# Performance work log

Hardware: AMD Instinct MI355X
Metric: run time of the kernel (lower is better)

The kernel has to match this reference:

```python
import jax, jax.numpy as jnp
import numpy as np

H = 16  # n_heads


def _ln(x, g, b, eps=1e-5):
    m = x.mean(-1, keepdims=True)
    v = ((x - m) ** 2).mean(-1, keepdims=True)
    return (x - m) / jnp.sqrt(v + eps) * g + b


def setup_inputs() -> dict:
    key = jax.random.key(0)
    ks = jax.random.split(key, 10)
    b, lq, d, dff, L = 2, 1024, 1024, 4096, 4
    s = 0.02
    return {
        "x": jax.random.normal(ks[0], (b, lq, d), jnp.float32),
        "memory_bank": jax.random.normal(ks[1], (L, b, lq, d), jnp.float32),
        "attn_mask": jax.random.bernoulli(ks[2], 0.3, (b, lq, lq)),
        "ln1_g": jnp.ones((d,), jnp.float32),
        "ln1_b": jnp.zeros((d,), jnp.float32),
        "Wq": jax.random.normal(ks[3], (d, d), jnp.float32) * s,
        "Wk": jax.random.normal(ks[4], (d, d), jnp.float32) * s,
        "Wv": jax.random.normal(ks[5], (d, d), jnp.float32) * s,
        "Wo": jax.random.normal(ks[6], (d, d), jnp.float32) * s,
        "ln2_g": jnp.ones((d,), jnp.float32),
        "ln2_b": jnp.zeros((d,), jnp.float32),
        "W1": jax.random.normal(ks[7], (d, dff), jnp.float32) * s,
        "b1": jnp.zeros((dff,), jnp.float32),
        "W2": jax.random.normal(ks[8], (dff, d), jnp.float32) * s,
        "b2": jnp.zeros((d,), jnp.float32),
    }


def reference(x, memory_bank, attn_mask, ln1_g, ln1_b, Wq, Wk, Wv, Wo,
              ln2_g, ln2_b, W1, b1, W2, b2):
    # x: [b, lq, d]; memory_bank: [L, b, lk, d]; attn_mask: [b, lq, lk] bool (True = masked)
    b, lq, d = x.shape
    dh = d // H
    # preprocess_attn: LayerNorm (eval mode -> dropouts are identity)
    q = _ln(x, ln1_g, ln1_b)
    # grow memory bank with current normalized input
    mem = jnp.concatenate([memory_bank, q[None]], axis=0)  # [L+1, b, lk, d]
    L, _, lk, _ = mem.shape
    # projections (bias-free); key/value projected per layer then flattened over (L, lk)
    pq = (q @ Wq).reshape(b, lq, H, dh).transpose(0, 2, 1, 3) * (dh ** -0.5)  # [b,h,lq,dh]
    pk = (mem @ Wk).transpose(1, 0, 2, 3).reshape(b, L * lk, H, dh).transpose(0, 2, 1, 3)
    pv = (mem @ Wv).transpose(1, 0, 2, 3).reshape(b, L * lk, H, dh).transpose(0, 2, 1, 3)
    scores = jnp.einsum('bhqd,bhkd->bhqk', pq, pk)           # [b,h,lq,L*lk]
    scores = scores.reshape(b, H, lq, L, lk)
    scores = jnp.where(attn_mask[:, None, :, None, :], -jnp.inf, scores)
    attn = jax.nn.softmax(scores.reshape(b, H, lq, L * lk), axis=-1)
    ctx = jnp.einsum('bhqk,bhkd->bhqd', attn, pv)            # [b,h,lq,dh]
    ctx = ctx.transpose(0, 2, 1, 3).reshape(b, lq, d)
    attn_out = ctx @ Wo
    # postprocess_attn: residual add
    x2 = x + attn_out
    # FFN: LayerNorm -> Linear -> ReLU -> Linear -> residual
    f = _ln(x2, ln2_g, ln2_b)
    f = jax.nn.relu(f @ W1 + b1) @ W2 + b2
    out = x2 + f
    return (out, mem)
```

## Files before the change

### kernel.cpp

```cpp
#include <hip/hip_runtime.h>
#include <hip/hip_bf16.h>

typedef __attribute__((ext_vector_type(8))) __bf16 bf16x8;
typedef __attribute__((ext_vector_type(4))) __bf16 bf16x4;
typedef __attribute__((ext_vector_type(4))) float f32x4;

#define MFMA16(a, b, c) __builtin_amdgcn_mfma_f32_16x16x32_bf16((a), (b), (c), 0, 0, 0)
#define LOG2E 1.4426950408889634f

static __device__ __forceinline__ float exp2_fast(float x) {
    float r; asm("v_exp_f32 %0, %1" : "=v"(r) : "v"(x)); return r;
}

__device__ __forceinline__ void gll16(const void* g, void* l) {
    __builtin_amdgcn_global_load_lds((const __attribute__((address_space(1))) void*)g,
                                     (__attribute__((address_space(3))) void*)l,
                                     16, 0, 0);
}

__global__ __launch_bounds__(256) void prep_kernel(const float* __restrict__ bank,
                                                   float* __restrict__ mem_out,
                                                   __bf16* __restrict__ membf,
                                                   const float* __restrict__ x,
                                                   const float* __restrict__ g,
                                                   const float* __restrict__ bta,
                                                   float* __restrict__ q_out,
                                                   __bf16* __restrict__ qbf) {
    __shared__ float rs[4], rs2[4];
    int blk = blockIdx.x;
    if (blk < 2048) {
        int i = blk * 256 + threadIdx.x;
        const float4* i4 = (const float4*)bank;
        float4* o4 = (float4*)mem_out;
        for (; i < 2097152; i += 2048 * 256) {
            float4 v = i4[i];
            o4[i] = v;
            if (membf) {
                bf16x4 ob = {(__bf16)v.x, (__bf16)v.y, (__bf16)v.z, (__bf16)v.w};
                ((bf16x4*)membf)[i] = ob;
            }
        }
    } else {
        int row = blk - 2048;
        const float4 v = ((const float4*)(x + (size_t)row * 1024))[threadIdx.x];
        float s = v.x + v.y + v.z + v.w;
        float s2 = v.x * v.x + v.y * v.y + v.z * v.z + v.w * v.w;
#pragma unroll
        for (int off = 1; off < 64; off <<= 1) {
            s += __shfl_xor(s, off);
            s2 += __shfl_xor(s2, off);
        }
        int wv = threadIdx.x >> 6;
        if ((threadIdx.x & 63) == 0) { rs[wv] = s; rs2[wv] = s2; }
        __syncthreads();
        s = rs[0] + rs[1] + rs[2] + rs[3];
        s2 = rs2[0] + rs2[1] + rs2[2] + rs2[3];
        float mean = s * (1.0f / 1024.0f);
        float var = s2 * (1.0f / 1024.0f) - mean * mean;
        float rstd = rsqrtf(var + 1e-5f);
        float4 gg = ((const float4*)g)[threadIdx.x];
        float4 bb = ((const float4*)bta)[threadIdx.x];
        float4 o;
        o.x = (v.x - mean) * rstd * gg.x + bb.x;
        o.y = (v.y - mean) * rstd * gg.y + bb.y;
        o.z = (v.z - mean) * rstd * gg.z + bb.z;
        o.w = (v.w - mean) * rstd * gg.w + bb.w;
        ((float4*)(q_out + (size_t)row * 1024))[threadIdx.x] = o;
        if (qbf) {
            bf16x4 ob = {(__bf16)o.x, (__bf16)o.y, (__bf16)o.z, (__bf16)o.w};
            ((bf16x4*)(qbf + (size_t)row * 1024))[threadIdx.x] = ob;
        }
    }
}

__global__ __launch_bounds__(256) void ln_kernel(const float* __restrict__ x,
                                                 const float* __restrict__ g,
                                                 const float* __restrict__ bta,
                                                 __bf16* __restrict__ outb) {
    int row = blockIdx.x;
    const float4 v = ((const float4*)(x + (size_t)row * 1024))[threadIdx.x];
    float s = v.x + v.y + v.z + v.w;
    float s2 = v.x * v.x + v.y * v.y + v.z * v.z + v.w * v.w;
#pragma unroll
    for (int off = 1; off < 64; off <<= 1) {
        s += __shfl_xor(s, off);
        s2 += __shfl_xor(s2, off);
    }
    __shared__ float rs[4], rs2[4];
    int wv = threadIdx.x >> 6;
    if ((threadIdx.x & 63) == 0) { rs[wv] = s; rs2[wv] = s2; }
    __syncthreads();
    s = rs[0] + rs[1] + rs[2] + rs[3];
    s2 = rs2[0] + rs2[1] + rs2[2] + rs2[3];
    float mean = s * (1.0f / 1024.0f);
    float var = s2 * (1.0f / 1024.0f) - mean * mean;
    float rstd = rsqrtf(var + 1e-5f);
    float4 gg = ((const float4*)g)[threadIdx.x];
    float4 bb = ((const float4*)bta)[threadIdx.x];
    bf16x4 ob;
    ob[0] = (__bf16)((v.x - mean) * rstd * gg.x + bb.x);
    ob[1] = (__bf16)((v.y - mean) * rstd * gg.y + bb.y);
    ob[2] = (__bf16)((v.z - mean) * rstd * gg.z + bb.z);
    ob[3] = (__bf16)((v.w - mean) * rstd * gg.w + bb.w);
    ((bf16x4*)(outb + (size_t)row * 1024))[threadIdx.x] = ob;
}

__device__ __forceinline__ void tr_body(const float* __restrict__ in, __bf16* __restrict__ out,
                                        int K, int N, int k0, int n0) {
    __shared__ float tile[32][33];
    int tx = threadIdx.x & 31, ty = threadIdx.x >> 5;
#pragma unroll
    for (int i = 0; i < 4; i++)
        tile[ty + i * 8][tx] = in[(size_t)(k0 + ty + i * 8) * N + n0 + tx];
    __syncthreads();
#pragma unroll
    for (int i = 0; i < 4; i++)
        out[(size_t)(n0 + ty + i * 8) * K + k0 + tx] = (__bf16)tile[tx][ty + i * 8];
}

__global__ __launch_bounds__(256) void tr_early(const float* __restrict__ Wq,
                                                const float* __restrict__ Wk,
                                                const float* __restrict__ Wv,
                                                __bf16* __restrict__ Wq_t,
                                                __bf16* __restrict__ Wkv_t) {
    int w = blockIdx.x;
    int sel = w >> 10, within = w & 1023;
    const float* in = (sel == 0) ? Wq : ((sel == 1) ? Wk : Wv);
    __bf16* out = (sel == 0) ? Wq_t : (Wkv_t + (size_t)(sel - 1) * 1048576);
    tr_body(in, out, 1024, 1024, (within >> 5) * 32, (within & 31) * 32);
}

__global__ __launch_bounds__(256) void tr_late(const float* __restrict__ Wo,
                                               const float* __restrict__ W1,
                                               const float* __restrict__ W2,
                                               __bf16* __restrict__ Wo_t,
                                               __bf16* __restrict__ W1_t,
                                               __bf16* __restrict__ W2_t) {
    int w = blockIdx.x;
    const float* in;
    __bf16* out;
    int K, N, k0, n0;
    if (w < 1024) {
        in = Wo; out = Wo_t; K = 1024; N = 1024; n0 = (w & 31) * 32; k0 = (w >> 5) * 32;
    } else if (w < 5120) {
        int v = w - 1024;
        in = W1; out = W1_t; K = 1024; N = 4096; n0 = (v & 127) * 32; k0 = (v >> 7) * 32;
    } else {
        int v = w - 5120;
        in = W2; out = W2_t; K = 4096; N = 1024; n0 = (v & 31) * 32; k0 = (v >> 5) * 32;
    }
    tr_body(in, out, K, N, k0, n0);
}

template <int EPI, bool ABF16>
__device__ __forceinline__ void gemm_core(const void* __restrict__ Av,
                                          const __bf16* __restrict__ Bt,
                                          void* __restrict__ Cout,
                                          const float* __restrict__ bias,
                                          const float* __restrict__ res,
                                          int N, int lda, int ldb, int klen,
                                          float scale, int bm, int bn) {
    constexpr int LDA = ABF16 ? 32 : 40;
    __shared__ __bf16 As[128 * LDA];
    __shared__ __bf16 Bs[128 * 32];

    int t = threadIdx.x;
    int lane = t & 63, wave = t >> 6;
    int wm = (wave >> 1) * 64, wn = (wave & 1) * 64;
    int l16 = lane & 15, l4 = lane >> 4;

    f32x4 acc[4][4];
#pragma unroll
    for (int m = 0; m < 4; m++)
#pragma unroll
        for (int n = 0; n < 4; n++) acc[m][n] = (f32x4){0.f, 0.f, 0.f, 0.f};

    int srow = t >> 2;
    int scol = (t & 3) * 8;
    int ar = t >> 1, ak = (t & 1) * 16;
    const __bf16* Ab = (const __bf16*)Av;
    const float* Af = (const float*)Av;

    for (int k0 = 0; k0 < klen; k0 += 32) {
        gll16(Bt + (size_t)(bn + srow) * ldb + (k0 + scol), &Bs[wave * 512]);
        gll16(Bt + (size_t)(bn + 64 + srow) * ldb + (k0 + scol), &Bs[2048 + wave * 512]);
        if constexpr (ABF16) {
            gll16(Ab + (size_t)(bm + srow) * lda + (k0 + scol), &As[wave * 512]);
            gll16(Ab + (size_t)(bm + 64 + srow) * lda + (k0 + scol), &As[2048 + wave * 512]);
        } else {
            const float* ap = Af + (size_t)(bm + ar) * lda + k0 + ak;
            float4 f0 = ((const float4*)ap)[0];
            float4 f1 = ((const float4*)ap)[1];
            float4 f2 = ((const float4*)ap)[2];
            float4 f3 = ((const float4*)ap)[3];
            float ta[16] = {f0.x, f0.y, f0.z, f0.w, f1.x, f1.y, f1.z, f1.w,
                            f2.x, f2.y, f2.z, f2.w, f3.x, f3.y, f3.z, f3.w};
            bf16x8 v0, v1;
#pragma unroll
            for (int j = 0; j < 8; j++) { v0[j] = (__bf16)ta[j]; v1[j] = (__bf16)ta[j + 8]; }
            *(bf16x8*)&As[ar * 40 + ak] = v0;
            *(bf16x8*)&As[ar * 40 + ak + 8] = v1;
        }
        __syncthreads();

        bf16x8 af[4], bfr[4];
#pragma unroll
        for (int m = 0; m < 4; m++) af[m] = *(const bf16x8*)&As[(wm + m * 16 + l16) * LDA + l4 * 8];
#pragma unroll
        for (int n = 0; n < 4; n++) bfr[n] = *(const bf16x8*)&Bs[(wn + n * 16 + l16) * 32 + l4 * 8];
#pragma unroll
        for (int m = 0; m < 4; m++)
#pragma unroll
            for (int n = 0; n < 4; n++) acc[m][n] = MFMA16(af[m], bfr[n], acc[m][n]);
        __syncthreads();
    }

#pragma unroll
    for (int m = 0; m < 4; m++) {
#pragma unroll
        for (int r = 0; r < 4; r++) {
            int row = bm + wm + m * 16 + l4 * 4 + r;
#pragma unroll
            for (int n = 0; n < 4; n++) {
                int col = bn + wn + n * 16 + l16;
                float c = acc[m][n][r];
                size_t idx = (size_t)row * N + col;
                if (EPI == 0) {
                    ((__bf16*)Cout)[idx] = (__bf16)(c * scale);
                } else if (EPI == 1) {
                    ((float*)Cout)[idx] = c + res[idx];
                } else if (EPI == 2) {
                    ((__bf16*)Cout)[idx] = (__bf16)fmaxf(c + bias[col], 0.0f);
                } else if (EPI == 3) {
                    ((float*)Cout)[idx] = c + bias[col] + res[idx];
                } else {
                    ((float*)Cout)[idx] = c;
                }
            }
        }
    }
}

template <int EPI, bool ABF16>
__global__ __launch_bounds__(256) void gemm_bt(const void* __restrict__ Av,
                                               const __bf16* __restrict__ Bt,
                                               void* __restrict__ Cout,
                                               const float* __restrict__ bias,
                                               const float* __restrict__ res,
                                               int N, int K, float scale, int nbx) {
    int q = gridDim.x >> 3;
    int swz = (blockIdx.x & 7) * q + (blockIdx.x >> 3);
    int bn = (swz % nbx) * 128;
    int bm = (swz / nbx) * 128;
    gemm_core<EPI, ABF16>(Av, Bt, Cout, bias, res, N, K, K, K, scale, bm, bn);
}

template <bool ABF16>
__global__ __launch_bounds__(256) void gemm_proj(const void* __restrict__ Akv,
                                                 const __bf16* __restrict__ Wkv_t,
                                                 __bf16* __restrict__ PKV,
                                                 const void* __restrict__ Aq,
                                                 const __bf16* __restrict__ Wq_t,
                                                 __bf16* __restrict__ Pq) {
    int q = gridDim.x >> 3;
    int swz = (blockIdx.x & 7) * q + (blockIdx.x >> 3);
    const void* A;
    const __bf16* B;
    __bf16* C;
    int N, bm, bn;
    float sc;
    if (swz < 1280) {
        A = Akv; B = Wkv_t; C = PKV; N = 2048; sc = 1.0f;
        bn = (swz & 15) * 128; bm = (swz >> 4) * 128;
    } else {
        int p = swz - 1280;
        A = Aq; B = Wq_t; C = Pq; N = 1024; sc = 0.125f * LOG2E;
        bn = (p & 7) * 128; bm = (p >> 3) * 128;
    }
    gemm_core<0, ABF16>(A, B, C, nullptr, nullptr, N, 1024, 1024, 1024, sc, bm, bn);
}

__global__ __launch_bounds__(256) void gemm_w2(const __bf16* __restrict__ h1,
                                               const __bf16* __restrict__ W2_t,
                                               float* __restrict__ pc0,
                                               float* __restrict__ pc1) {
    int q = gridDim.x >> 3;
    int swz = (blockIdx.x & 7) * q + (blockIdx.x >> 3);
    int half = swz >> 7;
    int p = swz & 127;
    int bn = (p & 7) * 128, bm = (p >> 3) * 128;
    int koff = half * 2048;
    gemm_core<4, true>(h1 + koff, W2_t + koff, half ? pc1 : pc0, nullptr, nullptr,
                       1024, 4096, 4096, 2048, 1.0f, bm, bn);
}

__global__ __launch_bounds__(256) void w2comb(const float* __restrict__ pc0,
                                              const float* __restrict__ pc1,
                                              const float* __restrict__ b2,
                                              const float* __restrict__ x2,
                                              float* __restrict__ out) {
    int i = blockIdx.x * 256 + threadIdx.x;
    float4 a = ((const float4*)pc0)[i];
    float4 b = ((const float4*)pc1)[i];
    float4 r = ((const float4*)x2)[i];
    float4 bb = ((const float4*)b2)[i & 255];
    float4 o;
    o.x = a.x + b.x + r.x + bb.x;
    o.y = a.y + b.y + r.y + bb.y;
    o.z = a.z + b.z + r.z + bb.z;
    o.w = a.w + b.w + r.w + bb.w;
    ((float4*)out)[i] = o;
}

#define LKV 5120
#define KHALF 2560
#define CK 64
#define NCH 40
__global__ __launch_bounds__(512, 4) void attn_kernel(const __bf16* __restrict__ Pq,
                                                      const __bf16* __restrict__ PKV,
                                                      const unsigned char* __restrict__ mask,
                                                      __bf16* __restrict__ ctx) {
    int bh = blockIdx.x;
    int b = bh >> 4, h = bh & 15;
    int wave = threadIdx.x >> 6, lane = threadIdx.x & 63;
    int grp = wave >> 2, wv = wave & 3;
    int l16 = lane & 15, l4 = lane >> 4;
    int q0 = blockIdx.y * 64 + wv * 16;

    __shared__ __bf16 Ks[2][64][72];
    __shared__ __bf16 Vt[2][64][72];
    __shared__ __bf16 Ps[8][16][72];

    const f32x4 fzero = {0.f, 0.f, 0.f, 0.f};

    bf16x8 qf[2];
    {
        const __bf16* pqrow = Pq + (size_t)(b * 1024 + q0 + l16) * 1024 + h * 64;
        qf[0] = *(const bf16x8*)(pqrow + l4 * 8);
        qf[1] = *(const bf16x8*)(pqrow + 32 + l4 * 8);
    }

    f32x4 accT[4];
#pragma unroll
    for (int n = 0; n < 4; n++) accT[n] = fzero;
    float m = 0.0f;
    float lsum = 0.0f;

    const unsigned char* mrow_p = mask + (size_t)b * (1024u * 1024u) + (size_t)(q0 + l16) * 1024;

    int tl = threadIdx.x & 255;
    int skey = tl >> 2;
    int sd0 = (tl & 3) << 4;
    int kgbase = grp * KHALF;

    bf16x8 rk0, rk1, rv0, rv1;
    unsigned int mk[4], mkn[4];
    {
        int kg = kgbase + skey;
        int lidx = kg >> 10, i = kg & 1023;
        size_t off = ((size_t)(lidx * 2048 + b * 1024 + i) << 11) + h * 64 + sd0;
        rk0 = *(const bf16x8*)(PKV + off);
        rk1 = *(const bf16x8*)(PKV + off + 8);
        rv0 = *(const bf16x8*)(PKV + off + 1024);
        rv1 = *(const bf16x8*)(PKV + off + 1032);
        int kloc = kgbase & 1023;
#pragma unroll
        for (int tile = 0; tile < 4; tile++)
            mk[tile] = *(const unsigned int*)(mrow_p + kloc + tile * 16 + l4 * 4);
    }

    for (int t = 0; t < NCH; t++) {
        *(bf16x8*)&Ks[grp][skey][sd0] = rk0;
        *(bf16x8*)&Ks[grp][skey][sd0 + 8] = rk1;
#pragma unroll
        for (int j = 0; j < 8; j++) {
            int row = sd0 + j;
            Vt[grp][row][skey ^ ((row >> 3) << 3)] = rv0[j];
            int row2 = sd0 + 8 + j;
            Vt[grp][row2][skey ^ ((row2 >> 3) << 3)] = rv1[j];
        }
        __syncthreads();

        if (t + 1 < NCH) {
            int kg = kgbase + (t + 1) * CK + skey;
            int lidx = kg >> 10, i = kg & 1023;
            size_t off = ((size_t)(lidx * 2048 + b * 1024 + i) << 11) + h * 64 + sd0;
            rk0 = *(const bf16x8*)(PKV + off);
            rk1 = *(const bf16x8*)(PKV + off + 8);
            rv0 = *(const bf16x8*)(PKV + off + 1024);
            rv1 = *(const bf16x8*)(PKV + off + 1032);
            int kloc = (kgbase + (t + 1) * CK) & 1023;
#pragma unroll
            for (int tile = 0; tile < 4; tile++)
                mkn[tile] = *(const unsigned int*)(mrow_p + kloc + tile * 16 + l4 * 4);
        }

        f32x4 s[4];
        __builtin_amdgcn_s_setprio(1);
#pragma unroll
        for (int tile = 0; tile < 4; tile++) {
            bf16x8 ka = *(const bf16x8*)&Ks[grp][tile * 16 + l16][l4 * 8];
            bf16x8 kb = *(const bf16x8*)&Ks[grp][tile * 16 + l16][32 + l4 * 8];
            f32x4 sz = fzero;
            sz = MFMA16(ka, qf[0], sz);
            sz = MFMA16(kb, qf[1], sz);
            s[tile] = sz;
        }
        __builtin_amdgcn_s_setprio(0);

        float pa = fmaxf(fmaxf(s[0][0], s[0][1]), fmaxf(s[0][2], s[0][3]));
        float pb = fmaxf(fmaxf(s[1][0], s[1][1]), fmaxf(s[1][2], s[1][3]));
        float pc = fmaxf(fmaxf(s[2][0], s[2][1]), fmaxf(s[2][2], s[2][3]));
        float pd = fmaxf(fmaxf(s[3][0], s[3][1]), fmaxf(s[3][2], s[3][3]));
        float pmax = fmaxf(fmaxf(pa, pb), fmaxf(pc, pd));
        pmax = fmaxf(pmax, __shfl_xor(pmax, 16));
        pmax = fmaxf(pmax, __shfl_xor(pmax, 32));
        if (__builtin_expect(pmax > m + 8.0f, 0)) {
            float sc = exp2_fast(m - pmax);
            lsum *= sc;
#pragma unroll
            for (int n = 0; n < 4; n++) accT[n] *= sc;
            m = pmax;
        }
        float psum = 0.0f;
#pragma unroll
        for (int tile = 0; tile < 4; tile++) {
            bf16x4 pk_;
#pragma unroll
            for (int r = 0; r < 4; r++) {
                float e = exp2_fast(s[tile][r] - m);
                e = ((mk[tile] >> (r * 8)) & 255u) ? 0.0f : e;
                psum += e;
                pk_[r] = (__bf16)e;
            }
            *(bf16x4*)&Ps[wave][l16][tile * 16 + l4 * 4] = pk_;
        }
        lsum += psum;
#pragma unroll
        for (int tile = 0; tile < 4; tile++) mk[tile] = mkn[tile];

        __builtin_amdgcn_s_setprio(1);
#pragma unroll
        for (int kk = 0; kk < 2; kk++) {
            bf16x8 pf = *(const bf16x8*)&Ps[wave][l16][kk * 32 + l4 * 8];
#pragma unroll
            for (int n = 0; n < 4; n++) {
                int row = n * 16 + l16;
                int colblk = (kk * 32 + l4 * 8) ^ ((row >> 3) << 3);
                bf16x8 vf = *(const bf16x8*)&Vt[grp][row][colblk];
                accT[n] = MFMA16(vf, pf, accT[n]);
            }
        }
        __builtin_amdgcn_s_setprio(0);
        __syncthreads();
    }

    lsum += __shfl_xor(lsum, 16);
    lsum += __shfl_xor(lsum, 32);

    float* exAcc = (float*)&Ks[0][0][0];
    float* exM = (float*)&Vt[0][0][0];
    float* exL = exM + 64;
    if (grp == 1) {
#pragma unroll
        for (int n = 0; n < 4; n++)
            *(f32x4*)&exAcc[(wv * 16 + l16) * 68 + n * 16 + l4 * 4] = accT[n];
        if (l4 == 0) { exM[wv * 16 + l16] = m; exL[wv * 16 + l16] = lsum; }
    }
    __syncthreads();
    if (grp == 0) {
        int qi = wv * 16 + l16;
        float m1 = exM[qi], l1 = exL[qi];
        float M = fmaxf(m, m1);
        float e0 = exp2_fast(m - M), e1 = exp2_fast(m1 - M);
        float inv = 1.0f / (lsum * e0 + l1 * e1);
        __bf16* crow = ctx + ((size_t)(b * 1024 + q0 + l16) << 10) + h * 64;
#pragma unroll
        for (int n = 0; n < 4; n++) {
            f32x4 a1 = *(const f32x4*)&exAcc[qi * 68 + n * 16 + l4 * 4];
            bf16x4 o;
#pragma unroll
            for (int r = 0; r < 4; r++) o[r] = (__bf16)((accT[n][r] * e0 + a1[r] * e1) * inv);
            *(bf16x4*)&crow[n * 16 + l4 * 4] = o;
        }
    }
}

extern "C" void kernel_launch(void* const* d_in, const int* in_sizes, int n_in,
                              void* d_out, int out_size, void* d_ws, size_t ws_size,
                              hipStream_t stream) {
    const float* x = (const float*)d_in[0];
    const float* memory_bank = (const float*)d_in[1];
    const unsigned char* attn_mask = (const unsigned char*)d_in[2];
    const float* ln1_g = (const float*)d_in[3];
    const float* ln1_b = (const float*)d_in[4];
    const float* Wq = (const float*)d_in[5];
    const float* Wk = (const float*)d_in[6];
    const float* Wv = (const float*)d_in[7];
    const float* Wo = (const float*)d_in[8];
    const float* ln2_g = (const float*)d_in[9];
    const float* ln2_b = (const float*)d_in[10];
    const float* W1 = (const float*)d_in[11];
    const float* b1 = (const float*)d_in[12];
    const float* W2 = (const float*)d_in[13];
    const float* b2 = (const float*)d_in[14];

    float* out = (float*)d_out;
    float* mem_out = out + 2097152;
    float* q_out = mem_out + 4 * 2097152;

    char* ws = (char*)d_ws;
    bool big = ws_size >= (70ull << 20);

    __bf16* PKV = (__bf16*)ws;
    __bf16 *Pq, *Wq_t, *Wkv_t, *ctx, *membf = nullptr, *qbf = nullptr;
    if (big) {
        membf = (__bf16*)(ws + (40ull << 20));
        qbf = membf + (size_t)8192 * 1024;
        Wq_t = (__bf16*)(ws + (60ull << 20));
        Wkv_t = (__bf16*)(ws + (62ull << 20));
        Pq = (__bf16*)(ws + (66ull << 20));
        ctx = (__bf16*)(ws + (60ull << 20));
    } else {
        Pq = (__bf16*)(ws + (40ull << 20));
        Wq_t = (__bf16*)(ws + (44ull << 20));
        Wkv_t = (__bf16*)(ws + (46ull << 20));
        ctx = (__bf16*)(ws + (44ull << 20));
    }
    __bf16* Wo_t = (__bf16*)ws;
    __bf16* W1_t = (__bf16*)(ws + (2ull << 20));
    __bf16* W2_t = (__bf16*)(ws + (10ull << 20));
    float* x2 = (float*)(ws + (18ull << 20));
    __bf16* fln = (__bf16*)(ws + (26ull << 20));
    __bf16* h1 = (__bf16*)(ws + (30ull << 20));
    float* pc0 = (float*)(ws + (46ull << 20));
    float* pc1 = (float*)(ws + (54ull << 20));

    prep_kernel<<<4096, 256, 0, stream>>>(memory_bank, mem_out, membf, x, ln1_g, ln1_b,
                                          q_out, qbf);
    tr_early<<<3072, 256, 0, stream>>>(Wq, Wk, Wv, Wq_t, Wkv_t);

    if (big)
        gemm_proj<true><<<1408, 256, 0, stream>>>(membf, Wkv_t, PKV, qbf, Wq_t, Pq);
    else
        gemm_proj<false><<<1408, 256, 0, stream>>>(mem_out, Wkv_t, PKV, q_out, Wq_t, Pq);

    attn_kernel<<<dim3(32, 16), 512, 0, stream>>>(Pq, PKV, attn_mask, ctx);

    tr_late<<<9216, 256, 0, stream>>>(Wo, W1, W2, Wo_t, W1_t, W2_t);

    gemm_bt<1, true><<<128, 256, 0, stream>>>(ctx, Wo_t, x2, nullptr, x, 1024, 1024, 1.0f, 8);
    ln_kernel<<<2048, 256, 0, stream>>>(x2, ln2_g, ln2_b, fln);
    gemm_bt<2, true><<<512, 256, 0, stream>>>(fln, W1_t, h1, b1, nullptr, 4096, 1024, 1.0f, 32);
    if (big) {
        gemm_w2<<<256, 256, 0, stream>>>(h1, W2_t, pc0, pc1);
        w2comb<<<2048, 256, 0, stream>>>(pc0, pc1, b2, x2, out);
    } else {
        gemm_bt<3, true><<<128, 256, 0, stream>>>(h1, W2_t, out, b2, x2, 1024, 4096, 1.0f, 8);
    }
}
```

Baseline: 301.7 us.

## Double-buffer attention K/V tiles with XOR swizzle and split-K the Wo GEMM

The attention kernel now keeps two LDS buffers for K and transposed V. The next chunk is written to LDS while the current one is consumed, so only one barrier per iteration is needed instead of two. Padding is replaced by XOR swizzles on the K, V and P tiles to avoid bank conflicts, and the global pointer advance is made incremental. The Wo projection is split into two K-halves writing fp32 partials, which a generalized combine kernel adds with the residual. This doubles the Wo grid for better CU occupancy but adds an extra pass over memory.

```diff
diff --git a/kernel.cpp b/kernel.cpp
--- a/kernel.cpp
+++ b/kernel.cpp
@@ -294,21 +294,38 @@
                        1024, 4096, 4096, 2048, 1.0f, bm, bn);
 }
 
-__global__ __launch_bounds__(256) void w2comb(const float* __restrict__ pc0,
-                                              const float* __restrict__ pc1,
-                                              const float* __restrict__ b2,
-                                              const float* __restrict__ x2,
-                                              float* __restrict__ out) {
+__global__ __launch_bounds__(256) void gemm_wo(const __bf16* __restrict__ ctx,
+                                               const __bf16* __restrict__ Wo_t,
+                                               float* __restrict__ pc0,
+                                               float* __restrict__ pc1) {
+    int q = gridDim.x >> 3;
+    int swz = (blockIdx.x & 7) * q + (blockIdx.x >> 3);
+    int half = swz >> 7;
+    int p = swz & 127;
+    int bn = (p & 7) * 128, bm = (p >> 3) * 128;
+    int koff = half * 512;
+    gemm_core<4, true>(ctx + koff, Wo_t + koff, half ? pc1 : pc0, nullptr, nullptr,
+                       1024, 1024, 1024, 512, 1.0f, bm, bn);
+}
+
+__global__ __launch_bounds__(256) void comb_kernel(const float* __restrict__ pc0,
+                                                   const float* __restrict__ pc1,
+                                                   const float* __restrict__ bias,
+                                                   const float* __restrict__ res,
+                                                   float* __restrict__ out) {
     int i = blockIdx.x * 256 + threadIdx.x;
     float4 a = ((const float4*)pc0)[i];
     float4 b = ((const float4*)pc1)[i];
-    float4 r = ((const float4*)x2)[i];
-    float4 bb = ((const float4*)b2)[i & 255];
+    float4 r = ((const float4*)res)[i];
     float4 o;
-    o.x = a.x + b.x + r.x + bb.x;
-    o.y = a.y + b.y + r.y + bb.y;
-    o.z = a.z + b.z + r.z + bb.z;
-    o.w = a.w + b.w + r.w + bb.w;
+    o.x = a.x + b.x + r.x;
+    o.y = a.y + b.y + r.y;
+    o.z = a.z + b.z + r.z;
+    o.w = a.w + b.w + r.w;
+    if (bias) {
+        float4 bb = ((const float4*)bias)[i & 255];
+        o.x += bb.x; o.y += bb.y; o.z += bb.z; o.w += bb.w;
+    }
     ((float4*)out)[i] = o;
 }
 
@@ -316,6 +333,8 @@
 #define KHALF 2560
 #define CK 64
 #define NCH 40
+#define KSW(r, c) ((c) ^ (((r) & 7) << 3))
+#define VSW(r, c) ((c) ^ ((((r) >> 3) & 7) << 3))
 __global__ __launch_bounds__(512, 4) void attn_kernel(const __bf16* __restrict__ Pq,
                                                       const __bf16* __restrict__ PKV,
                                                       const unsigned char* __restrict__ mask,
@@ -327,9 +346,9 @@
     int l16 = lane & 15, l4 = lane >> 4;
     int q0 = blockIdx.y * 64 + wv * 16;
 
-    __shared__ __bf16 Ks[2][64][72];
-    __shared__ __bf16 Vt[2][64][72];
-    __shared__ __bf16 Ps[8][16][72];
+    __shared__ __bf16 Ks[2][2][64][64];
+    __shared__ __bf16 Vt[2][2][64][64];
+    __shared__ __bf16 Ps[8][16][64];
 
     const f32x4 fzero = {0.f, 0.f, 0.f, 0.f};
 
@@ -353,54 +372,73 @@
     int sd0 = (tl & 3) << 4;
     int kgbase = grp * KHALF;
 
+    int kmod = kgbase & 1023;
+    const __bf16* pkv = PKV + (((size_t)((kgbase >> 10) * 2048 + b * 1024 + kmod + skey)) << 11)
+                        + h * 64 + sd0;
     bf16x8 rk0, rk1, rv0, rv1;
     unsigned int mk[4], mkn[4];
-    {
-        int kg = kgbase + skey;
-        int lidx = kg >> 10, i = kg & 1023;
-        size_t off = ((size_t)(lidx * 2048 + b * 1024 + i) << 11) + h * 64 + sd0;
-        rk0 = *(const bf16x8*)(PKV + off);
-        rk1 = *(const bf16x8*)(PKV + off + 8);
-        rv0 = *(const bf16x8*)(PKV + off + 1024);
-        rv1 = *(const bf16x8*)(PKV + off + 1032);
-        int kloc = kgbase & 1023;
-#pragma unroll
-        for (int tile = 0; tile < 4; tile++)
-            mk[tile] = *(const unsigned int*)(mrow_p + kloc + tile * 16 + l4 * 4);
-    }
+
+    rk0 = *(const bf16x8*)(pkv);
+    rk1 = *(const bf16x8*)(pkv + 8);
+    rv0 = *(const bf16x8*)(pkv + 1024);
+    rv1 = *(const bf16x8*)(pkv + 1032);
+    { int st = (kmod + CK >= 1024) ? (CK + 1024) : CK; kmod = (kmod + CK) & 1023; pkv += (size_t)st << 11; }
+    int kloc0 = kgbase & 1023;
+#pragma unroll
+    for (int tile = 0; tile < 4; tile++)
+        mk[tile] = *(const unsigned int*)(mrow_p + kloc0 + tile * 16 + l4 * 4);
+    int kloc_m = (kloc0 + CK) & 1023;
+
+    *(bf16x8*)&Ks[grp][0][skey][KSW(skey, sd0)] = rk0;
+    *(bf16x8*)&Ks[grp][0][skey][KSW(skey, sd0 + 8)] = rk1;
+#pragma unroll
+    for (int j = 0; j < 8; j++) {
+        int r1 = sd0 + j, r2 = sd0 + 8 + j;
+        Vt[grp][0][r1][VSW(r1, skey)] = rv0[j];
+        Vt[grp][0][r2][VSW(r2, skey)] = rv1[j];
+    }
+    rk0 = *(const bf16x8*)(pkv);
+    rk1 = *(const bf16x8*)(pkv + 8);
+    rv0 = *(const bf16x8*)(pkv + 1024);
+    rv1 = *(const bf16x8*)(pkv + 1032);
+    { int st = (kmod + CK >= 1024) ? (CK + 1024) : CK; kmod = (kmod + CK) & 1023; pkv += (size_t)st << 11; }
 
     for (int t = 0; t < NCH; t++) {
-        *(bf16x8*)&Ks[grp][skey][sd0] = rk0;
-        *(bf16x8*)&Ks[grp][skey][sd0 + 8] = rk1;
-#pragma unroll
-        for (int j = 0; j < 8; j++) {
-            int row = sd0 + j;
-            Vt[grp][row][skey ^ ((row >> 3) << 3)] = rv0[j];
-            int row2 = sd0 + 8 + j;
-            Vt[grp][row2][skey ^ ((row2 >> 3) << 3)] = rv1[j];
-        }
+        int cb = t & 1, nb = cb ^ 1;
         __syncthreads();
-
         if (t + 1 < NCH) {
-            int kg = kgbase + (t + 1) * CK + skey;
-            int lidx = kg >> 10, i = kg & 1023;
-            size_t off = ((size_t)(lidx * 2048 + b * 1024 + i) << 11) + h * 64 + sd0;
-            rk0 = *(const bf16x8*)(PKV + off);
-            rk1 = *(const bf16x8*)(PKV + off + 8);
-            rv0 = *(const bf16x8*)(PKV + off + 1024);
-            rv1 = *(const bf16x8*)(PKV + off + 1032);
-            int kloc = (kgbase + (t + 1) * CK) & 1023;
+            *(bf16x8*)&Ks[grp][nb][skey][KSW(skey, sd0)] = rk0;
+            *(bf16x8*)&Ks[grp][nb][skey][KSW(skey, sd0 + 8)] = rk1;
+#pragma unroll
+            for (int j = 0; j < 8; j++) {
+                int r1 = sd0 + j, r2 = sd0 + 8 + j;
+                Vt[grp][nb][r1][VSW(r1, skey)] = rv0[j];
+                Vt[grp][nb][r2][VSW(r2, skey)] = rv1[j];
+            }
+        }
+        if (t + 2 < NCH) {
+            rk0 = *(const bf16x8*)(pkv);
+            rk1 = *(const bf16x8*)(pkv + 8);
+            rv0 = *(const bf16x8*)(pkv + 1024);
+            rv1 = *(const bf16x8*)(pkv + 1032);
+            int st = (kmod + CK >= 1024) ? (CK + 1024) : CK;
+            kmod = (kmod + CK) & 1023;
+            pkv += (size_t)st << 11;
+        }
+        if (t + 1 < NCH) {
 #pragma unroll
             for (int tile = 0; tile < 4; tile++)
-                mkn[tile] = *(const unsigned int*)(mrow_p + kloc + tile * 16 + l4 * 4);
+                mkn[tile] = *(const unsigned int*)(mrow_p + kloc_m + tile * 16 + l4 * 4);
+            kloc_m = (kloc_m + CK) & 1023;
         }
 
         f32x4 s[4];
         __builtin_amdgcn_s_setprio(1);
 #pragma unroll
         for (int tile = 0; tile < 4; tile++) {
-            bf16x8 ka = *(const bf16x8*)&Ks[grp][tile * 16 + l16][l4 * 8];
-            bf16x8 kb = *(const bf16x8*)&Ks[grp][tile * 16 + l16][32 + l4 * 8];
+            int row = tile * 16 + l16;
+            bf16x8 ka = *(const bf16x8*)&Ks[grp][cb][row][KSW(row, l4 * 8)];
+            bf16x8 kb = *(const bf16x8*)&Ks[grp][cb][row][KSW(row, 32 + l4 * 8)];
             f32x4 sz = fzero;
             sz = MFMA16(ka, qf[0], sz);
             sz = MFMA16(kb, qf[1], sz);
@@ -433,7 +471,7 @@
                 psum += e;
                 pk_[r] = (__bf16)e;
             }
-            *(bf16x4*)&Ps[wave][l16][tile * 16 + l4 * 4] = pk_;
+            *(bf16x4*)&Ps[wave][l16][KSW(l16, tile * 16 + l4 * 4)] = pk_;
         }
         lsum += psum;
 #pragma unroll
@@ -442,29 +480,28 @@
         __builtin_amdgcn_s_setprio(1);
 #pragma unroll
         for (int kk = 0; kk < 2; kk++) {
-            bf16x8 pf = *(const bf16x8*)&Ps[wave][l16][kk * 32 + l4 * 8];
+            bf16x8 pf = *(const bf16x8*)&Ps[wave][l16][KSW(l16, kk * 32 + l4 * 8)];
 #pragma unroll
             for (int n = 0; n < 4; n++) {
                 int row = n * 16 + l16;
-                int colblk = (kk * 32 + l4 * 8) ^ ((row >> 3) << 3);
-                bf16x8 vf = *(const bf16x8*)&Vt[grp][row][colblk];
+                bf16x8 vf = *(const bf16x8*)&Vt[grp][cb][row][VSW(row, kk * 32 + l4 * 8)];
                 accT[n] = MFMA16(vf, pf, accT[n]);
             }
         }
         __builtin_amdgcn_s_setprio(0);
-        __syncthreads();
     }
 
     lsum += __shfl_xor(lsum, 16);
     lsum += __shfl_xor(lsum, 32);
 
-    float* exAcc = (float*)&Ks[0][0][0];
-    float* exM = (float*)&Vt[0][0][0];
+    __syncthreads();
+    float* exAcc = (float*)&Ks[0][0][0][0];
+    float* exM = (float*)&Vt[0][0][0][0];
     float* exL = exM + 64;
     if (grp == 1) {
 #pragma unroll
         for (int n = 0; n < 4; n++)
-            *(f32x4*)&exAcc[(wv * 16 + l16) * 68 + n * 16 + l4 * 4] = accT[n];
+            *(f32x4*)&exAcc[(wv * 16 + l16) * 64 + n * 16 + l4 * 4] = accT[n];
         if (l4 == 0) { exM[wv * 16 + l16] = m; exL[wv * 16 + l16] = lsum; }
     }
     __syncthreads();
@@ -477,7 +514,7 @@
         __bf16* crow = ctx + ((size_t)(b * 1024 + q0 + l16) << 10) + h * 64;
 #pragma unroll
         for (int n = 0; n < 4; n++) {
-            f32x4 a1 = *(const f32x4*)&exAcc[qi * 68 + n * 16 + l4 * 4];
+            f32x4 a1 = *(const f32x4*)&exAcc[qi * 64 + n * 16 + l4 * 4];
             bf16x4 o;
 #pragma unroll
             for (int r = 0; r < 4; r++) o[r] = (__bf16)((accT[n][r] * e0 + a1[r] * e1) * inv);
@@ -533,6 +570,8 @@
     float* x2 = (float*)(ws + (18ull << 20));
     __bf16* fln = (__bf16*)(ws + (26ull << 20));
     __bf16* h1 = (__bf16*)(ws + (30ull << 20));
+    float* wo_pc0 = (float*)(ws + (30ull << 20));
+    float* wo_pc1 = (float*)(ws + (38ull << 20));
     float* pc0 = (float*)(ws + (46ull << 20));
     float* pc1 = (float*)(ws + (54ull << 20));
 
@@ -549,12 +588,17 @@
 
     tr_late<<<9216, 256, 0, stream>>>(Wo, W1, W2, Wo_t, W1_t, W2_t);
 
-    gemm_bt<1, true><<<128, 256, 0, stream>>>(ctx, Wo_t, x2, nullptr, x, 1024, 1024, 1.0f, 8);
+    if (big) {
+        gemm_wo<<<256, 256, 0, stream>>>(ctx, Wo_t, wo_pc0, wo_pc1);
+        comb_kernel<<<2048, 256, 0, stream>>>(wo_pc0, wo_pc1, nullptr, x, x2);
+    } else {
+        gemm_bt<1, true><<<128, 256, 0, stream>>>(ctx, Wo_t, x2, nullptr, x, 1024, 1024, 1.0f, 8);
+    }
     ln_kernel<<<2048, 256, 0, stream>>>(x2, ln2_g, ln2_b, fln);
     gemm_bt<2, true><<<512, 256, 0, stream>>>(fln, W1_t, h1, b1, nullptr, 4096, 1024, 1.0f, 32);
     if (big) {
         gemm_w2<<<256, 256, 0, stream>>>(h1, W2_t, pc0, pc1);
-        w2comb<<<2048, 256, 0, stream>>>(pc0, pc1, b2, x2, out);
+        comb_kernel<<<2048, 256, 0, stream>>>(pc0, pc1, b2, x2, out);
     } else {
         gemm_bt<3, true><<<128, 256, 0, stream>>>(h1, W2_t, out, b2, x2, 1024, 4096, 1.0f, 8);
     }
```

New measurement: 302.3 us. No clear change (+0.2%).
